# Kernel tuning notes

Hardware: AMD Instinct MI355X
Metric: run time of the kernel (lower is better)

The kernel has to match this reference:

```python
import jax, jax.numpy as jnp
import numpy as np

DEPTH = 10
WIDTH = 128
DIM = 2
N = 1_048_576


def setup_inputs() -> dict:
    key = jax.random.key(0)
    ks = jax.random.split(key, 14)
    x = jax.random.normal(ks[0], (N, DIM), jnp.float32)

    # Orthogonal init for the invertible 1x1 convs (QR of a random matrix),
    # matching Invertible1x1Conv.__init__.
    rng = np.random.default_rng(0)
    conv_w = np.stack([np.linalg.qr(rng.standard_normal((DIM, DIM)))[0]
                       for _ in range(DEPTH)]).astype(np.float32)

    def nrm(k, shape, sc=0.1):
        return sc * jax.random.normal(k, shape, jnp.float32)

    return dict(
        x=x,
        an_scale=jnp.exp(nrm(ks[1], (DEPTH, DIM))),          # outer actnorm, positive
        an_bias=nrm(ks[2], (DEPTH, DIM)),
        conv_w=jnp.asarray(conv_w),                           # [D, 2, 2]
        fc1_w=nrm(ks[3], (DEPTH, WIDTH, DIM // 2), 1.0),      # Linear(1, 128)
        fc1_b=nrm(ks[4], (DEPTH, WIDTH)),
        an1_scale=jnp.exp(nrm(ks[5], (DEPTH, WIDTH))),
        an1_bias=nrm(ks[6], (DEPTH, WIDTH)),
        fc2_w=nrm(ks[7], (DEPTH, WIDTH, WIDTH)),              # Linear(128, 128)
        fc2_b=nrm(ks[8], (DEPTH, WIDTH)),
        an2_scale=jnp.exp(nrm(ks[9], (DEPTH, WIDTH))),
        an2_bias=nrm(ks[10], (DEPTH, WIDTH)),
        fc3_w=nrm(ks[11], (DEPTH, DIM, WIDTH)),               # Linear(128, 2)
        fc3_b=nrm(ks[12], (DEPTH, DIM)),
        log_scale_factor=nrm(ks[13], (DEPTH, DIM)),
    )


def reference(x, an_scale, an_bias, conv_w, fc1_w, fc1_b, an1_scale, an1_bias,
              fc2_w, fc2_b, an2_scale, an2_bias, fc3_w, fc3_b, log_scale_factor):
    z = x
    logdet = jnp.zeros((x.shape[0],), x.dtype)
    half = DIM // 2
    for i in range(DEPTH):  # fixed depth=10, structurally distinct params
        # --- Actnorm ---
        z = (z - an_bias[i]) / an_scale[i]
        logdet = logdet - jnp.sum(jnp.log(jnp.abs(an_scale[i])))
        # --- Invertible 1x1 conv ---
        logdet = logdet + jnp.linalg.slogdet(conv_w[i])[1]
        z = z @ conv_w[i].T
        # --- Affine coupling (inner actnorms are already initialized) ---
        z_a, z_b = z[:, :half], z[:, half:]
        h = jax.nn.relu((z_b @ fc1_w[i].T + fc1_b[i] - an1_bias[i]) / an1_scale[i])
        h = jax.nn.relu((h @ fc2_w[i].T + fc2_b[i] - an2_bias[i]) / an2_scale[i])
        h = (h @ fc3_w[i].T + fc3_b[i]) * jnp.exp(log_scale_factor[i])  # [N, 2]
        t = h[:, 0::2]                         # [N, 1]
        s = jax.nn.sigmoid(h[:, 1::2] + 2.0)   # [N, 1]
        z = jnp.concatenate([s * z_a + t, z_b], axis=1)
        logdet = logdet + jnp.sum(jnp.log(s), axis=1)
    return z, logdet
```

## Files before the change

kernel.cpp:

```cpp
#include <hip/hip_runtime.h>
#include <math.h>


constexpr int kDepth = 10;
constexpr int kWidth = 128;
constexpr float kVMin = -24.0f;
constexpr float kVMax =  24.0f;

__global__ void prep_kernel(
    const float* __restrict__ an_scale, const float* __restrict__ an_bias,
    const float* __restrict__ conv_w,
    const float* __restrict__ fc1_w, const float* __restrict__ fc1_b,
    const float* __restrict__ an1_scale, const float* __restrict__ an1_bias,
    const float* __restrict__ fc2_w, const float* __restrict__ fc2_b,
    const float* __restrict__ an2_scale, const float* __restrict__ an2_bias,
    const float* __restrict__ fc3_b, const float* __restrict__ lsf,
    float* __restrict__ meta, float* __restrict__ kv,
    float* __restrict__ CG, float* __restrict__ CB)
{
  __shared__ float sWT[128 * 129];
  __shared__ float sVs[128], sG[128], sB[128];
  __shared__ float sGs[128], sBs[128];
  __shared__ int   sOrd[128];

  const int l = blockIdx.x;
  const int t = threadIdx.x;

  const float* wl = fc2_w + (size_t)l * kWidth * kWidth;
#pragma unroll 8
  for (int fi = t; fi < 128 * 128; fi += 256) {
    const int k = fi >> 7, j = fi & 127;
    sWT[j * 129 + k] = wl[fi];
  }

  if (t < 128) {
    const float s1 = an1_scale[l*kWidth + t];
    const float g = fc1_w[l*kWidth + t] / s1;
    const float b = (fc1_b[l*kWidth + t] - an1_bias[l*kWidth + t]) / s1;
    float vs, sg;
    if (g > 0.0f)      { vs = -b / g; sg =  1.0f; }
    else if (g < 0.0f) { vs = -b / g; sg = -1.0f; }
    else               { vs = (b > 0.0f) ? -1e30f : 1e30f; sg = (b > 0.0f) ? 1.0f : 0.0f; }
    sG[t] = g; sB[t] = b; sVs[t] = vs;
    sGs[t] = sg * g; sBs[t] = sg * b;
  }
  __syncthreads();

  if (t < 128) {
    const float my = sVs[t];
    int r = 0;
    const float4* vs4 = (const float4*)sVs;
#pragma unroll
    for (int i4 = 0; i4 < 32; ++i4) {
      float4 o = vs4[i4];
      const int ib = i4 * 4;
      r += (o.x < my) || (o.x == my && ib + 0 < t);
      r += (o.y < my) || (o.y == my && ib + 1 < t);
      r += (o.z < my) || (o.z == my && ib + 2 < t);
      r += (o.w < my) || (o.w == my && ib + 3 < t);
    }
    sOrd[r] = t;
  }
  __syncthreads();

  if (t < 128) {
    kv[l*128 + t] = sVs[sOrd[t]];

    float cg = 0.0f;
    float cb = fc2_b[l*kWidth + t] - an2_bias[l*kWidth + t];
    const float4* g4 = (const float4*)sG;
    const float4* b4 = (const float4*)sB;
#pragma unroll
    for (int j4 = 0; j4 < 32; ++j4) {
      float4 G = g4[j4], B = b4[j4];
      const int j = j4 * 4;
      float w0 = sWT[(j + 0) * 129 + t];
      float w1 = sWT[(j + 1) * 129 + t];
      float w2 = sWT[(j + 2) * 129 + t];
      float w3 = sWT[(j + 3) * 129 + t];
      if (G.x < 0.0f) { cg = fmaf(G.x, w0, cg); cb = fmaf(B.x, w0, cb); }
      if (G.y < 0.0f) { cg = fmaf(G.y, w1, cg); cb = fmaf(B.y, w1, cb); }
      if (G.z < 0.0f) { cg = fmaf(G.z, w2, cg); cb = fmaf(B.z, w2, cb); }
      if (G.w < 0.0f) { cg = fmaf(G.w, w3, cg); cb = fmaf(B.w, w3, cb); }
    }

    const size_t base = (size_t)l * 129 * 128;
    int4 J = ((const int4*)sOrd)[0];
    float w0 = sWT[J.x * 129 + t];
    float w1 = sWT[J.y * 129 + t];
    float w2 = sWT[J.z * 129 + t];
    float w3 = sWT[J.w * 129 + t];
#pragma unroll 1
    for (int c = 0; c < 32; ++c) {
      const int4 Jc = J;
      const float v0 = w0, v1 = w1, v2 = w2, v3 = w3;
      if (c + 1 < 32) {
        J = ((const int4*)sOrd)[c + 1];
        w0 = sWT[J.x * 129 + t];
        w1 = sWT[J.y * 129 + t];
        w2 = sWT[J.z * 129 + t];
        w3 = sWT[J.w * 129 + t];
      }
      const int p = c * 4;
      CG[base + (size_t)(p + 0) * 128 + t] = cg;
      CB[base + (size_t)(p + 0) * 128 + t] = cb;
      cg = fmaf(sGs[Jc.x], v0, cg); cb = fmaf(sBs[Jc.x], v0, cb);
      CG[base + (size_t)(p + 1) * 128 + t] = cg;
      CB[base + (size_t)(p + 1) * 128 + t] = cb;
      cg = fmaf(sGs[Jc.y], v1, cg); cb = fmaf(sBs[Jc.y], v1, cb);
      CG[base + (size_t)(p + 2) * 128 + t] = cg;
      CB[base + (size_t)(p + 2) * 128 + t] = cb;
      cg = fmaf(sGs[Jc.z], v2, cg); cb = fmaf(sBs[Jc.z], v2, cb);
      CG[base + (size_t)(p + 3) * 128 + t] = cg;
      CB[base + (size_t)(p + 3) * 128 + t] = cb;
      cg = fmaf(sGs[Jc.w], v3, cg); cb = fmaf(sBs[Jc.w], v3, cb);
    }
    CG[base + (size_t)128 * 128 + t] = cg;
    CB[base + (size_t)128 * 128 + t] = cb;
  }

  if (t == 0) {
    meta[16 + l*4 + 0] = expf(lsf[l*2 + 0]);
    meta[16 + l*4 + 1] = expf(lsf[l*2 + 1]);
    meta[16 + l*4 + 2] = fc3_b[l*2 + 0];
    meta[16 + l*4 + 3] = fc3_b[l*2 + 1];

    const float sx = an_scale[l*2+0], sy = an_scale[l*2+1];
    const float bx = an_bias[l*2+0],  by = an_bias[l*2+1];
    const float* cw = conv_w + l*4;
    const float m00 = cw[0]/sx, m01 = cw[1]/sy;
    const float m10 = cw[2]/sx, m11 = cw[3]/sy;
    meta[64 + l*8 + 0] = m00;
    meta[64 + l*8 + 1] = m01;
    meta[64 + l*8 + 2] = m10;
    meta[64 + l*8 + 3] = m11;
    meta[64 + l*8 + 4] = -(m00*bx + m01*by);
    meta[64 + l*8 + 5] = -(m10*bx + m11*by);
  }
  if (l == 0 && t == 0) {
    float cst = 0.0f;
    for (int i = 0; i < kDepth; ++i) {
      cst -= logf(fabsf(an_scale[i*2+0]));
      cst -= logf(fabsf(an_scale[i*2+1]));
      const float* cw = conv_w + i * 4;
      float det = cw[0]*cw[3] - cw[1]*cw[2];
      cst += logf(fabsf(det));
    }
    meta[0] = cst;
  }
}

__global__ __launch_bounds__(256) void table_kernel(
    const float* __restrict__ an2_scale,
    const float* __restrict__ fc3_w,
    const float* __restrict__ meta, const float* __restrict__ kv,
    const float* __restrict__ CG, const float* __restrict__ CB,
    int tabN, float4* __restrict__ tab)
{
  __shared__ float sKz[128], sKw[128], sKv[128];
  __shared__ int   sP[64];

  const int bpl   = tabN >> 6;
  const int l     = blockIdx.x / bpl;
  const int node0 = (blockIdx.x % bpl) * 64;
  const int t     = threadIdx.x;
  const float dv  = (kVMax - kVMin) / (float)(tabN - 1);

  if (t < 128) {
    const float si = 1.0f / an2_scale[l*kWidth + t];
    sKz[t] = fc3_w[l*2*kWidth + t] * si;
    sKw[t] = fc3_w[l*2*kWidth + kWidth + t] * si;
    sKv[t] = kv[l*128 + t];
  }
  __syncthreads();

  if (t < 64) {
    const float v = kVMin + dv * (float)(node0 + t);
    int p = 0;
    const float4* kv4 = (const float4*)sKv;
#pragma unroll
    for (int m = 0; m < 32; ++m) {
      float4 K = kv4[m];
      p += (K.x < v) + (K.y < v) + (K.z < v) + (K.w < v);
    }
    sP[t] = p;
  }
  __syncthreads();

  const int node = t >> 2, kq = t & 3;
  const int p = sP[node];
  const float v = kVMin + dv * (float)(node0 + node);

  const float4* cg4 = (const float4*)(CG + ((size_t)l*129 + p) * 128 + kq*32);
  const float4* cb4 = (const float4*)(CB + ((size_t)l*129 + p) * 128 + kq*32);
  const float4* kz4 = (const float4*)sKz + kq*8;
  const float4* kw4 = (const float4*)sKw + kq*8;

  float o0 = 0.f, o1 = 0.f, p0 = 0.f, p1 = 0.f;
#pragma unroll
  for (int c = 0; c < 8; ++c) {
    float4 G = cg4[c], B = cb4[c], Z = kz4[c], W = kw4[c];
    float raw, h, dd;
    raw = fmaf(v, G.x, B.x); h = fmaxf(raw, 0.f); dd = (raw > 0.f) ? G.x : 0.f;
    o0 = fmaf(h, Z.x, o0); o1 = fmaf(h, W.x, o1); p0 = fmaf(dd, Z.x, p0); p1 = fmaf(dd, W.x, p1);
    raw = fmaf(v, G.y, B.y); h = fmaxf(raw, 0.f); dd = (raw > 0.f) ? G.y : 0.f;
    o0 = fmaf(h, Z.y, o0); o1 = fmaf(h, W.y, o1); p0 = fmaf(dd, Z.y, p0); p1 = fmaf(dd, W.y, p1);
    raw = fmaf(v, G.z, B.z); h = fmaxf(raw, 0.f); dd = (raw > 0.f) ? G.z : 0.f;
    o0 = fmaf(h, Z.z, o0); o1 = fmaf(h, W.z, o1); p0 = fmaf(dd, Z.z, p0); p1 = fmaf(dd, W.z, p1);
    raw = fmaf(v, G.w, B.w); h = fmaxf(raw, 0.f); dd = (raw > 0.f) ? G.w : 0.f;
    o0 = fmaf(h, Z.w, o0); o1 = fmaf(h, W.w, o1); p0 = fmaf(dd, Z.w, p0); p1 = fmaf(dd, W.w, p1);
  }

  o0 += __shfl_xor(o0, 1); o0 += __shfl_xor(o0, 2);
  o1 += __shfl_xor(o1, 1); o1 += __shfl_xor(o1, 2);
  p0 += __shfl_xor(p0, 1); p0 += __shfl_xor(p0, 2);
  p1 += __shfl_xor(p1, 1); p1 += __shfl_xor(p1, 2);

  if (kq == 0) {
    const float E0  = meta[16 + l*4 + 0];
    const float E1  = meta[16 + l*4 + 1];
    const float b30 = meta[16 + l*4 + 2];
    const float b31 = meta[16 + l*4 + 3];
    tab[(size_t)l * tabN + node0 + node] =
        make_float4((o0 + b30) * E0, p0 * E0, (o1 + b31) * E1, p1 * E1);
  }
}

__global__ __launch_bounds__(1024) void flow_apply_kernel(
    const float* __restrict__ x,
    const float4* __restrict__ tab, const float* __restrict__ meta,
    int tabN,
    float* __restrict__ out_z, float* __restrict__ out_ld, int n)
{
  __shared__ float4 sTab[2][2048];

  const int t = threadIdx.x;
  const int base = blockIdx.x * 2048;
  const int s0 = base + t;
  const int s1 = base + 1024 + t;
  const bool ok0 = s0 < n, ok1 = s1 < n;

  float2 z0 = ok0 ? reinterpret_cast<const float2*>(x)[s0] : make_float2(0.f, 0.f);
  float2 z1 = ok1 ? reinterpret_cast<const float2*>(x)[s1] : make_float2(0.f, 0.f);
  const float ldc = meta[0];
  float ld0 = ldc, ld1 = ldc;

  const float dv = (kVMax - kVMin) / (float)(tabN - 1);
  const float inv_dv = (float)(tabN - 1) / (kVMax - kVMin);
  const float offv = -kVMin * inv_dv;
  const float qmax = (float)(tabN - 1);
  constexpr float kLog2e = 1.44269504088896340736f;
  constexpr float kLn2   = 0.69314718055994530942f;

  {
    float4 ra = tab[t];
    float4 rb = tab[t + 1024];
    sTab[0][t] = ra;
    sTab[0][t + 1024] = rb;
  }
  __syncthreads();

  int cur = 0;
#pragma unroll 1
  for (int i = 0; i < kDepth; ++i) {
    float4 ra, rb;
    if (i + 1 < kDepth) {
      const float4* tn = tab + (size_t)(i + 1) * tabN;
      ra = tn[t];
      rb = tn[t + 1024];
    }

    const float m00 = meta[64 + i*8 + 0], m01 = meta[64 + i*8 + 1];
    const float m10 = meta[64 + i*8 + 2], m11 = meta[64 + i*8 + 3];
    const float q0  = meta[64 + i*8 + 4], q1  = meta[64 + i*8 + 5];
    const float4* tl = sTab[cur];

#pragma unroll
    for (int c = 0; c < 2; ++c) {
      float2& z  = c ? z1 : z0;
      float&  ld = c ? ld1 : ld0;
      const float na = fmaf(m00, z.x, fmaf(m01, z.y, q0));
      const float nb = fmaf(m10, z.x, fmaf(m11, z.y, q1));
      float xq = fmaf(nb, inv_dv, offv);
      xq = fminf(fmaxf(xq, 0.0f), qmax);
      const int qn = (int)(xq + 0.5f);
      const float4 e = tl[qn];
      const float vn = fmaf((float)qn, dv, kVMin);
      const float f = nb - vn;
      const float tt = fmaf(f, e.y, e.x);
      const float uu = fmaf(f, e.w, e.z);
      const float arg = uu + 2.0f;
      const float ev = __builtin_amdgcn_exp2f(arg * -kLog2e);
      const float den = 1.0f + ev;
      const float s = __builtin_amdgcn_rcpf(den);
      ld = fmaf(-kLn2, __builtin_amdgcn_logf(den), ld);
      z.x = fmaf(s, na, tt);
      z.y = nb;
    }

    __syncthreads();
    if (i + 1 < kDepth) {
      sTab[cur ^ 1][t] = ra;
      sTab[cur ^ 1][t + 1024] = rb;
    }
    __syncthreads();
    cur ^= 1;
  }

  if (ok0) {
    reinterpret_cast<float2*>(out_z)[s0] = z0;
    out_ld[s0] = ld0;
  }
  if (ok1) {
    reinterpret_cast<float2*>(out_z)[s1] = z1;
    out_ld[s1] = ld1;
  }
}

extern "C" void kernel_launch(void* const* d_in, const int* in_sizes, int n_in,
                              void* d_out, int out_size, void* d_ws, size_t ws_size,
                              hipStream_t stream) {
  const float* x         = (const float*)d_in[0];
  const float* an_scale  = (const float*)d_in[1];
  const float* an_bias   = (const float*)d_in[2];
  const float* conv_w    = (const float*)d_in[3];
  const float* fc1_w     = (const float*)d_in[4];
  const float* fc1_b     = (const float*)d_in[5];
  const float* an1_scale = (const float*)d_in[6];
  const float* an1_bias  = (const float*)d_in[7];
  const float* fc2_w     = (const float*)d_in[8];
  const float* fc2_b     = (const float*)d_in[9];
  const float* an2_scale = (const float*)d_in[10];
  const float* an2_bias  = (const float*)d_in[11];
  const float* fc3_w     = (const float*)d_in[12];
  const float* fc3_b     = (const float*)d_in[13];
  const float* lsf       = (const float*)d_in[14];

  const int n = in_sizes[0] / 2;

  const size_t metaF = 256, kvF = (size_t)kDepth * 128;
  const size_t cF = (size_t)kDepth * 129 * 128;
  const size_t headF = metaF + kvF + 2 * cF;
  int tabN = 2048;
  while (tabN > 512 &&
         headF * 4 + (size_t)kDepth * tabN * sizeof(float4) > ws_size) {
    tabN >>= 1;
  }
  float* meta = (float*)d_ws;
  float* kv   = meta + metaF;
  float* CG   = kv + kvF;
  float* CB   = CG + cF;
  float4* tab = (float4*)(CB + cF);

  prep_kernel<<<kDepth, 256, 0, stream>>>(
      an_scale, an_bias, conv_w, fc1_w, fc1_b, an1_scale, an1_bias,
      fc2_w, fc2_b, an2_scale, an2_bias, fc3_b, lsf,
      meta, kv, CG, CB);

  table_kernel<<<kDepth * (tabN / 64), 256, 0, stream>>>(
      an2_scale, fc3_w, meta, kv, CG, CB, tabN, tab);

  const int blocks = (n + 2047) / 2048;
  flow_apply_kernel<<<blocks, 1024, 0, stream>>>(
      x, tab, meta, tabN, (float*)d_out, (float*)d_out + (size_t)2 * n, n);
}
```

Before: 44.45 us.

## Halve lookup table, split into float2 arrays, process four samples per thread

Cuts the per-layer lookup table from 2048 to 1024 entries and stores it as two float2 shared arrays instead of one float4 array. Each block now handles 4096 samples, four per thread, which halves the number of blocks and table loads per sample. This spreads the table-staging cost and barrier overhead over more work and reduces LDS traffic. In exchange, the coarser table interpolation loses accuracy, and fewer blocks with more registers per thread may lower occupancy.

```diff
diff --git a/kernel.cpp b/kernel.cpp
--- a/kernel.cpp
+++ b/kernel.cpp
@@ -232,18 +232,24 @@
     int tabN,
     float* __restrict__ out_z, float* __restrict__ out_ld, int n)
 {
-  __shared__ float4 sTab[2][2048];
+  __shared__ float2 sTU[2][1024];
+  __shared__ float2 sDT[2][1024];
 
   const int t = threadIdx.x;
-  const int base = blockIdx.x * 2048;
-  const int s0 = base + t;
-  const int s1 = base + 1024 + t;
-  const bool ok0 = s0 < n, ok1 = s1 < n;
-
-  float2 z0 = ok0 ? reinterpret_cast<const float2*>(x)[s0] : make_float2(0.f, 0.f);
-  float2 z1 = ok1 ? reinterpret_cast<const float2*>(x)[s1] : make_float2(0.f, 0.f);
+  const int base = blockIdx.x * 4096;
+
+  int   sid[4];
+  bool  ok[4];
+  float2 z[4];
+  float ldv[4];
   const float ldc = meta[0];
-  float ld0 = ldc, ld1 = ldc;
+#pragma unroll
+  for (int c = 0; c < 4; ++c) {
+    sid[c] = base + c * 1024 + t;
+    ok[c] = sid[c] < n;
+    z[c] = ok[c] ? reinterpret_cast<const float2*>(x)[sid[c]] : make_float2(0.f, 0.f);
+    ldv[c] = ldc;
+  }
 
   const float dv = (kVMax - kVMin) / (float)(tabN - 1);
   const float inv_dv = (float)(tabN - 1) / (kVMax - kVMin);
@@ -252,68 +258,63 @@
   constexpr float kLog2e = 1.44269504088896340736f;
   constexpr float kLn2   = 0.69314718055994530942f;
 
-  {
-    float4 ra = tab[t];
-    float4 rb = tab[t + 1024];
-    sTab[0][t] = ra;
-    sTab[0][t + 1024] = rb;
+  if (t < tabN) {
+    float4 e = tab[t];
+    sTU[0][t] = make_float2(e.x, e.z);
+    sDT[0][t] = make_float2(e.y, e.w);
   }
   __syncthreads();
 
   int cur = 0;
 #pragma unroll 1
   for (int i = 0; i < kDepth; ++i) {
-    float4 ra, rb;
-    if (i + 1 < kDepth) {
-      const float4* tn = tab + (size_t)(i + 1) * tabN;
-      ra = tn[t];
-      rb = tn[t + 1024];
-    }
+    float4 en = make_float4(0.f, 0.f, 0.f, 0.f);
+    if (i + 1 < kDepth && t < tabN)
+      en = tab[(size_t)(i + 1) * tabN + t];
 
     const float m00 = meta[64 + i*8 + 0], m01 = meta[64 + i*8 + 1];
     const float m10 = meta[64 + i*8 + 2], m11 = meta[64 + i*8 + 3];
     const float q0  = meta[64 + i*8 + 4], q1  = meta[64 + i*8 + 5];
-    const float4* tl = sTab[cur];
-
-#pragma unroll
-    for (int c = 0; c < 2; ++c) {
-      float2& z  = c ? z1 : z0;
-      float&  ld = c ? ld1 : ld0;
-      const float na = fmaf(m00, z.x, fmaf(m01, z.y, q0));
-      const float nb = fmaf(m10, z.x, fmaf(m11, z.y, q1));
+    const float2* tu = sTU[cur];
+    const float2* dt = sDT[cur];
+
+#pragma unroll
+    for (int c = 0; c < 4; ++c) {
+      const float na = fmaf(m00, z[c].x, fmaf(m01, z[c].y, q0));
+      const float nb = fmaf(m10, z[c].x, fmaf(m11, z[c].y, q1));
       float xq = fmaf(nb, inv_dv, offv);
       xq = fminf(fmaxf(xq, 0.0f), qmax);
       const int qn = (int)(xq + 0.5f);
-      const float4 e = tl[qn];
+      const float2 e  = tu[qn];
+      const float2 de = dt[qn];
       const float vn = fmaf((float)qn, dv, kVMin);
       const float f = nb - vn;
-      const float tt = fmaf(f, e.y, e.x);
-      const float uu = fmaf(f, e.w, e.z);
+      const float tt = fmaf(f, de.x, e.x);
+      const float uu = fmaf(f, de.y, e.y);
       const float arg = uu + 2.0f;
       const float ev = __builtin_amdgcn_exp2f(arg * -kLog2e);
       const float den = 1.0f + ev;
       const float s = __builtin_amdgcn_rcpf(den);
-      ld = fmaf(-kLn2, __builtin_amdgcn_logf(den), ld);
-      z.x = fmaf(s, na, tt);
-      z.y = nb;
+      ldv[c] = fmaf(-kLn2, __builtin_amdgcn_logf(den), ldv[c]);
+      z[c].x = fmaf(s, na, tt);
+      z[c].y = nb;
     }
 
     __syncthreads();
-    if (i + 1 < kDepth) {
-      sTab[cur ^ 1][t] = ra;
-      sTab[cur ^ 1][t + 1024] = rb;
+    if (i + 1 < kDepth && t < tabN) {
+      sTU[cur ^ 1][t] = make_float2(en.x, en.z);
+      sDT[cur ^ 1][t] = make_float2(en.y, en.w);
     }
     __syncthreads();
     cur ^= 1;
   }
 
-  if (ok0) {
-    reinterpret_cast<float2*>(out_z)[s0] = z0;
-    out_ld[s0] = ld0;
-  }
-  if (ok1) {
-    reinterpret_cast<float2*>(out_z)[s1] = z1;
-    out_ld[s1] = ld1;
+#pragma unroll
+  for (int c = 0; c < 4; ++c) {
+    if (ok[c]) {
+      reinterpret_cast<float2*>(out_z)[sid[c]] = z[c];
+      out_ld[sid[c]] = ldv[c];
+    }
   }
 }
 
@@ -341,8 +342,8 @@
   const size_t metaF = 256, kvF = (size_t)kDepth * 128;
   const size_t cF = (size_t)kDepth * 129 * 128;
   const size_t headF = metaF + kvF + 2 * cF;
-  int tabN = 2048;
-  while (tabN > 512 &&
+  int tabN = 1024;
+  while (tabN > 256 &&
          headF * 4 + (size_t)kDepth * tabN * sizeof(float4) > ws_size) {
     tabN >>= 1;
   }
@@ -360,7 +361,7 @@
   table_kernel<<<kDepth * (tabN / 64), 256, 0, stream>>>(
       an2_scale, fc3_w, meta, kv, CG, CB, tabN, tab);
 
-  const int blocks = (n + 2047) / 2048;
+  const int blocks = (n + 4095) / 4096;
   flow_apply_kernel<<<blocks, 1024, 0, stream>>>(
       x, tab, meta, tabN, (float*)d_out, (float*)d_out + (size_t)2 * n, n);
 }
```

New measurement: 45.32 us. About the same (+2.0%).

## Fuse table build into prep kernel and preload smaller bf16-packed tables

Applied to the files above, without the earlier changes.

Merges the prep and table-building kernels into one launch, with each depth block building its own table after a threadfence. This cuts the table from 2048 to 512 nodes and stores slopes as packed bf16, so all ten layers' tables fit in shared memory at once. That removes the per-layer double-buffered reload and its two barriers per layer in the apply kernel. In exchange, accuracy drops from the coarser grid and bf16 slopes, and the table build now runs on only ten blocks serially.

```diff
diff --git a/kernel.cpp b/kernel.cpp
--- a/kernel.cpp
+++ b/kernel.cpp
@@ -7,24 +7,30 @@
 constexpr float kVMin = -24.0f;
 constexpr float kVMax =  24.0f;
 
-__global__ void prep_kernel(
+__global__ __launch_bounds__(256) void prep_table_kernel(
     const float* __restrict__ an_scale, const float* __restrict__ an_bias,
     const float* __restrict__ conv_w,
     const float* __restrict__ fc1_w, const float* __restrict__ fc1_b,
     const float* __restrict__ an1_scale, const float* __restrict__ an1_bias,
     const float* __restrict__ fc2_w, const float* __restrict__ fc2_b,
     const float* __restrict__ an2_scale, const float* __restrict__ an2_bias,
-    const float* __restrict__ fc3_b, const float* __restrict__ lsf,
-    float* __restrict__ meta, float* __restrict__ kv,
-    float* __restrict__ CG, float* __restrict__ CB)
+    const float* __restrict__ fc3_w, const float* __restrict__ fc3_b,
+    const float* __restrict__ lsf,
+    int tabN,
+    float* __restrict__ meta,
+    float* __restrict__ CG, float* __restrict__ CB,
+    float4* __restrict__ tab)
 {
   __shared__ float sWT[128 * 129];
   __shared__ float sVs[128], sG[128], sB[128];
   __shared__ float sGs[128], sBs[128];
+  __shared__ float sKv[128], sKz[128], sKw[128];
   __shared__ int   sOrd[128];
+  __shared__ int   sP[64];
 
   const int l = blockIdx.x;
   const int t = threadIdx.x;
+  const float dv = (kVMax - kVMin) / (float)(tabN - 1);
 
   const float* wl = fc2_w + (size_t)l * kWidth * kWidth;
 #pragma unroll 8
@@ -43,6 +49,9 @@
     else               { vs = (b > 0.0f) ? -1e30f : 1e30f; sg = (b > 0.0f) ? 1.0f : 0.0f; }
     sG[t] = g; sB[t] = b; sVs[t] = vs;
     sGs[t] = sg * g; sBs[t] = sg * b;
+    const float si = 1.0f / an2_scale[l*kWidth + t];
+    sKz[t] = fc3_w[l*2*kWidth + t] * si;
+    sKw[t] = fc3_w[l*2*kWidth + kWidth + t] * si;
   }
   __syncthreads();
 
@@ -64,7 +73,7 @@
   __syncthreads();
 
   if (t < 128) {
-    kv[l*128 + t] = sVs[sOrd[t]];
+    sKv[t] = sVs[sOrd[t]];
 
     float cg = 0.0f;
     float cb = fc2_b[l*kWidth + t] - an2_bias[l*kWidth + t];
@@ -148,82 +157,75 @@
     }
     meta[0] = cst;
   }
+
+  __threadfence();
+  __syncthreads();
+
+  const float E0  = meta[16 + l*4 + 0];
+  const float E1  = meta[16 + l*4 + 1];
+  const float b30 = meta[16 + l*4 + 2];
+  const float b31 = meta[16 + l*4 + 3];
+
+#pragma unroll 1
+  for (int chunk = 0; chunk < (tabN >> 6); ++chunk) {
+    const int node0 = chunk * 64;
+
+    if (t < 64) {
+      const float v = kVMin + dv * (float)(node0 + t);
+      int p = 0;
+      const float4* kv4 = (const float4*)sKv;
+#pragma unroll
+      for (int m = 0; m < 32; ++m) {
+        float4 K = kv4[m];
+        p += (K.x < v) + (K.y < v) + (K.z < v) + (K.w < v);
+      }
+      sP[t] = p;
+    }
+    __syncthreads();
+
+    const int node = t >> 2, kq = t & 3;
+    const int p = sP[node];
+    const float v = kVMin + dv * (float)(node0 + node);
+
+    const float4* cg4 = (const float4*)(CG + ((size_t)l*129 + p) * 128 + kq*32);
+    const float4* cb4 = (const float4*)(CB + ((size_t)l*129 + p) * 128 + kq*32);
+    const float4* kz4 = (const float4*)sKz + kq*8;
+    const float4* kw4 = (const float4*)sKw + kq*8;
+
+    float o0 = 0.f, o1 = 0.f, p0 = 0.f, p1 = 0.f;
+#pragma unroll
+    for (int c = 0; c < 8; ++c) {
+      float4 G = cg4[c], B = cb4[c], Z = kz4[c], W = kw4[c];
+      float raw, h, dd;
+      raw = fmaf(v, G.x, B.x); h = fmaxf(raw, 0.f); dd = (raw > 0.f) ? G.x : 0.f;
+      o0 = fmaf(h, Z.x, o0); o1 = fmaf(h, W.x, o1); p0 = fmaf(dd, Z.x, p0); p1 = fmaf(dd, W.x, p1);
+      raw = fmaf(v, G.y, B.y); h = fmaxf(raw, 0.f); dd = (raw > 0.f) ? G.y : 0.f;
+      o0 = fmaf(h, Z.y, o0); o1 = fmaf(h, W.y, o1); p0 = fmaf(dd, Z.y, p0); p1 = fmaf(dd, W.y, p1);
+      raw = fmaf(v, G.z, B.z); h = fmaxf(raw, 0.f); dd = (raw > 0.f) ? G.z : 0.f;
+      o0 = fmaf(h, Z.z, o0); o1 = fmaf(h, W.z, o1); p0 = fmaf(dd, Z.z, p0); p1 = fmaf(dd, W.z, p1);
+      raw = fmaf(v, G.w, B.w); h = fmaxf(raw, 0.f); dd = (raw > 0.f) ? G.w : 0.f;
+      o0 = fmaf(h, Z.w, o0); o1 = fmaf(h, W.w, o1); p0 = fmaf(dd, Z.w, p0); p1 = fmaf(dd, W.w, p1);
+    }
+
+    o0 += __shfl_xor(o0, 1); o0 += __shfl_xor(o0, 2);
+    o1 += __shfl_xor(o1, 1); o1 += __shfl_xor(o1, 2);
+    p0 += __shfl_xor(p0, 1); p0 += __shfl_xor(p0, 2);
+    p1 += __shfl_xor(p1, 1); p1 += __shfl_xor(p1, 2);
+
+    if (kq == 0) {
+      tab[(size_t)l * tabN + node0 + node] =
+          make_float4((o0 + b30) * E0, p0 * E0, (o1 + b31) * E1, p1 * E1);
+    }
+    __syncthreads();
+  }
 }
 
-__global__ __launch_bounds__(256) void table_kernel(
-    const float* __restrict__ an2_scale,
-    const float* __restrict__ fc3_w,
-    const float* __restrict__ meta, const float* __restrict__ kv,
-    const float* __restrict__ CG, const float* __restrict__ CB,
-    int tabN, float4* __restrict__ tab)
-{
-  __shared__ float sKz[128], sKw[128], sKv[128];
-  __shared__ int   sP[64];
-
-  const int bpl   = tabN >> 6;
-  const int l     = blockIdx.x / bpl;
-  const int node0 = (blockIdx.x % bpl) * 64;
-  const int t     = threadIdx.x;
-  const float dv  = (kVMax - kVMin) / (float)(tabN - 1);
-
-  if (t < 128) {
-    const float si = 1.0f / an2_scale[l*kWidth + t];
-    sKz[t] = fc3_w[l*2*kWidth + t] * si;
-    sKw[t] = fc3_w[l*2*kWidth + kWidth + t] * si;
-    sKv[t] = kv[l*128 + t];
-  }
-  __syncthreads();
-
-  if (t < 64) {
-    const float v = kVMin + dv * (float)(node0 + t);
-    int p = 0;
-    const float4* kv4 = (const float4*)sKv;
-#pragma unroll
-    for (int m = 0; m < 32; ++m) {
-      float4 K = kv4[m];
-      p += (K.x < v) + (K.y < v) + (K.z < v) + (K.w < v);
-    }
-    sP[t] = p;
-  }
-  __syncthreads();
-
-  const int node = t >> 2, kq = t & 3;
-  const int p = sP[node];
-  const float v = kVMin + dv * (float)(node0 + node);
-
-  const float4* cg4 = (const float4*)(CG + ((size_t)l*129 + p) * 128 + kq*32);
-  const float4* cb4 = (const float4*)(CB + ((size_t)l*129 + p) * 128 + kq*32);
-  const float4* kz4 = (const float4*)sKz + kq*8;
-  const float4* kw4 = (const float4*)sKw + kq*8;
-
-  float o0 = 0.f, o1 = 0.f, p0 = 0.f, p1 = 0.f;
-#pragma unroll
-  for (int c = 0; c < 8; ++c) {
-    float4 G = cg4[c], B = cb4[c], Z = kz4[c], W = kw4[c];
-    float raw, h, dd;
-    raw = fmaf(v, G.x, B.x); h = fmaxf(raw, 0.f); dd = (raw > 0.f) ? G.x : 0.f;
-    o0 = fmaf(h, Z.x, o0); o1 = fmaf(h, W.x, o1); p0 = fmaf(dd, Z.x, p0); p1 = fmaf(dd, W.x, p1);
-    raw = fmaf(v, G.y, B.y); h = fmaxf(raw, 0.f); dd = (raw > 0.f) ? G.y : 0.f;
-    o0 = fmaf(h, Z.y, o0); o1 = fmaf(h, W.y, o1); p0 = fmaf(dd, Z.y, p0); p1 = fmaf(dd, W.y, p1);
-    raw = fmaf(v, G.z, B.z); h = fmaxf(raw, 0.f); dd = (raw > 0.f) ? G.z : 0.f;
-    o0 = fmaf(h, Z.z, o0); o1 = fmaf(h, W.z, o1); p0 = fmaf(dd, Z.z, p0); p1 = fmaf(dd, W.z, p1);
-    raw = fmaf(v, G.w, B.w); h = fmaxf(raw, 0.f); dd = (raw > 0.f) ? G.w : 0.f;
-    o0 = fmaf(h, Z.w, o0); o1 = fmaf(h, W.w, o1); p0 = fmaf(dd, Z.w, p0); p1 = fmaf(dd, W.w, p1);
-  }
-
-  o0 += __shfl_xor(o0, 1); o0 += __shfl_xor(o0, 2);
-  o1 += __shfl_xor(o1, 1); o1 += __shfl_xor(o1, 2);
-  p0 += __shfl_xor(p0, 1); p0 += __shfl_xor(p0, 2);
-  p1 += __shfl_xor(p1, 1); p1 += __shfl_xor(p1, 2);
-
-  if (kq == 0) {
-    const float E0  = meta[16 + l*4 + 0];
-    const float E1  = meta[16 + l*4 + 1];
-    const float b30 = meta[16 + l*4 + 2];
-    const float b31 = meta[16 + l*4 + 3];
-    tab[(size_t)l * tabN + node0 + node] =
-        make_float4((o0 + b30) * E0, p0 * E0, (o1 + b31) * E1, p1 * E1);
-  }
+__device__ __forceinline__ unsigned int pack_bf16(float a, float b) {
+  unsigned int ua = __float_as_uint(a);
+  unsigned int ub = __float_as_uint(b);
+  ua = (ua + 0x7FFFu + ((ua >> 16) & 1u)) >> 16;
+  ub = (ub + 0x7FFFu + ((ub >> 16) & 1u)) >> 16;
+  return ua | (ub << 16);
 }
 
 __global__ __launch_bounds__(1024) void flow_apply_kernel(
@@ -232,14 +234,21 @@
     int tabN,
     float* __restrict__ out_z, float* __restrict__ out_ld, int n)
 {
-  __shared__ float4 sTab[2][2048];
+  __shared__ float2       sTU[kDepth * 512];
+  __shared__ unsigned int sPK[kDepth * 512];
 
   const int t = threadIdx.x;
   const int base = blockIdx.x * 2048;
+
+  for (int j = t; j < kDepth * tabN; j += 1024) {
+    float4 e = tab[j];
+    sTU[j] = make_float2(e.x, e.z);
+    sPK[j] = pack_bf16(e.y, e.w);
+  }
+
   const int s0 = base + t;
   const int s1 = base + 1024 + t;
   const bool ok0 = s0 < n, ok1 = s1 < n;
-
   float2 z0 = ok0 ? reinterpret_cast<const float2*>(x)[s0] : make_float2(0.f, 0.f);
   float2 z1 = ok1 ? reinterpret_cast<const float2*>(x)[s1] : make_float2(0.f, 0.f);
   const float ldc = meta[0];
@@ -252,28 +261,15 @@
   constexpr float kLog2e = 1.44269504088896340736f;
   constexpr float kLn2   = 0.69314718055994530942f;
 
-  {
-    float4 ra = tab[t];
-    float4 rb = tab[t + 1024];
-    sTab[0][t] = ra;
-    sTab[0][t + 1024] = rb;
-  }
   __syncthreads();
 
-  int cur = 0;
 #pragma unroll 1
   for (int i = 0; i < kDepth; ++i) {
-    float4 ra, rb;
-    if (i + 1 < kDepth) {
-      const float4* tn = tab + (size_t)(i + 1) * tabN;
-      ra = tn[t];
-      rb = tn[t + 1024];
-    }
-
     const float m00 = meta[64 + i*8 + 0], m01 = meta[64 + i*8 + 1];
     const float m10 = meta[64 + i*8 + 2], m11 = meta[64 + i*8 + 3];
     const float q0  = meta[64 + i*8 + 4], q1  = meta[64 + i*8 + 5];
-    const float4* tl = sTab[cur];
+    const float2* tu = sTU + i * tabN;
+    const unsigned int* pk = sPK + i * tabN;
 
 #pragma unroll
     for (int c = 0; c < 2; ++c) {
@@ -284,11 +280,14 @@
       float xq = fmaf(nb, inv_dv, offv);
       xq = fminf(fmaxf(xq, 0.0f), qmax);
       const int qn = (int)(xq + 0.5f);
-      const float4 e = tl[qn];
+      const float2 e = tu[qn];
+      const unsigned int d = pk[qn];
+      const float dt = __uint_as_float(d << 16);
+      const float du = __uint_as_float(d & 0xFFFF0000u);
       const float vn = fmaf((float)qn, dv, kVMin);
       const float f = nb - vn;
-      const float tt = fmaf(f, e.y, e.x);
-      const float uu = fmaf(f, e.w, e.z);
+      const float tt = fmaf(f, dt, e.x);
+      const float uu = fmaf(f, du, e.y);
       const float arg = uu + 2.0f;
       const float ev = __builtin_amdgcn_exp2f(arg * -kLog2e);
       const float den = 1.0f + ev;
@@ -297,14 +296,6 @@
       z.x = fmaf(s, na, tt);
       z.y = nb;
     }
-
-    __syncthreads();
-    if (i + 1 < kDepth) {
-      sTab[cur ^ 1][t] = ra;
-      sTab[cur ^ 1][t + 1024] = rb;
-    }
-    __syncthreads();
-    cur ^= 1;
   }
 
   if (ok0) {
@@ -338,27 +329,23 @@
 
   const int n = in_sizes[0] / 2;
 
-  const size_t metaF = 256, kvF = (size_t)kDepth * 128;
+  const size_t metaF = 256;
   const size_t cF = (size_t)kDepth * 129 * 128;
-  const size_t headF = metaF + kvF + 2 * cF;
-  int tabN = 2048;
-  while (tabN > 512 &&
+  const size_t headF = metaF + 2 * cF;
+  int tabN = 512;
+  while (tabN > 128 &&
          headF * 4 + (size_t)kDepth * tabN * sizeof(float4) > ws_size) {
     tabN >>= 1;
   }
   float* meta = (float*)d_ws;
-  float* kv   = meta + metaF;
-  float* CG   = kv + kvF;
+  float* CG   = meta + metaF;
   float* CB   = CG + cF;
   float4* tab = (float4*)(CB + cF);
 
-  prep_kernel<<<kDepth, 256, 0, stream>>>(
+  prep_table_kernel<<<kDepth, 256, 0, stream>>>(
       an_scale, an_bias, conv_w, fc1_w, fc1_b, an1_scale, an1_bias,
-      fc2_w, fc2_b, an2_scale, an2_bias, fc3_b, lsf,
-      meta, kv, CG, CB);
-
-  table_kernel<<<kDepth * (tabN / 64), 256, 0, stream>>>(
-      an2_scale, fc3_w, meta, kv, CG, CB, tabN, tab);
+      fc2_w, fc2_b, an2_scale, an2_bias, fc3_w, fc3_b, lsf, tabN,
+      meta, CG, CB, tab);
 
   const int blocks = (n + 2047) / 2048;
   flow_apply_kernel<<<blocks, 1024, 0, stream>>>(
```

New measurement: 62.11 us. 39.7% more time.
